# Optimization experiments

Measured on AMD Instinct MI355X. Metric: run time of the kernel, lower is better.

Reference implementation:

```python
import jax, jax.numpy as jnp
import numpy as np

B, N, C, K = 2, 4096, 256, 64


def setup_inputs() -> dict:
    key = jax.random.key(0)
    k1, k2, k3, k4, k5, k6 = jax.random.split(key, 6)
    points = jax.random.normal(k1, (B, N, 3), dtype=jnp.float32)  # ~N(0,1) cloud
    point_features = jax.random.normal(k2, (B, N, C), dtype=jnp.float32)
    # proposals: centers inside the cloud, positive box dims, random yaw (unused by mask math)
    centers = jax.random.uniform(k3, (B, K, 3), minval=-1.0, maxval=1.0, dtype=jnp.float32)
    dims = jax.random.uniform(k4, (B, K, 3), minval=0.5, maxval=1.5, dtype=jnp.float32)
    ry = jax.random.uniform(k5, (B, K, 1), minval=-np.pi, maxval=np.pi, dtype=jnp.float32)
    proposals = jnp.concatenate([centers, dims, ry], axis=-1)  # (B,K,7)
    W1 = jax.random.normal(k6, (C, 256), dtype=jnp.float32) * (1.0 / np.sqrt(C))
    b1 = jnp.zeros((256,), dtype=jnp.float32)
    W2 = jax.random.normal(jax.random.fold_in(key, 7), (256, 256), dtype=jnp.float32) * (1.0 / 16.0)
    b2 = jnp.zeros((256,), dtype=jnp.float32)
    return {"points": points, "point_features": point_features, "proposals": proposals,
            "W1": W1, "b1": b1, "W2": W2, "b2": b2}


def reference(points, point_features, proposals, W1, b1, W2, b2):
    # points: (B,N,3), point_features: (B,N,C), proposals: (B,K,7)
    ctr = proposals[..., :3]                      # (B,K,3) cx,cy,cz
    half = proposals[..., 3:6] * 0.5              # (B,K,3) l/2,w/2,h/2
    lo = ctr - half                               # (B,K,3)
    hi = ctr + half
    # point-in-box mask (axis-aligned, strict inequalities as in source): (B,K,N)
    p = points[:, None, :, :]                     # (B,1,N,3)
    mask = jnp.all((p > lo[:, :, None, :]) & (p < hi[:, :, None, :]), axis=-1)
    any_in = jnp.any(mask, axis=-1)               # (B,K)
    # masked max-pool over points: (B,K,N,C) -> (B,K,C)
    neg_inf = jnp.asarray(-jnp.inf, point_features.dtype)
    masked = jnp.where(mask[..., None], point_features[:, None, :, :], neg_inf)
    pooled = jnp.max(masked, axis=2)
    pooled = jnp.where(any_in[..., None], pooled, 0.0)  # empty box -> zeros
    # fc: Linear(C,256) + ReLU + Linear(256,256) + ReLU
    h = jax.nn.relu(jnp.einsum('bkc,cd->bkd', pooled, W1) + b1)
    out = jax.nn.relu(jnp.einsum('bkd,de->bke', h, W2) + b2)
    return out
```

## Files before the change

### kernel.cpp

```cpp
#include <hip/hip_runtime.h>

#define Bn 2
#define Nn 4096
#define Cn 256
#define Kn 64
#define BK (Bn * Kn)
#define NSEG 8
#define SEGN (Nn / NSEG)
#define NB1 (BK * NSEG)
#define W1T 4
#define PAD1 (7 * W1T)

__device__ __forceinline__ float4 max4(float4 a, float4 b) {
    return make_float4(fmaxf(a.x, b.x), fmaxf(a.y, b.y),
                       fmaxf(a.z, b.z), fmaxf(a.w, b.w));
}

__global__ __launch_bounds__(256) void pool_seg_kernel(
    const float* __restrict__ points,
    const float* __restrict__ feats,
    const float* __restrict__ proposals,
    float* __restrict__ partial)
{
    const int blk  = blockIdx.x;
    const int bk   = blk >> 3;
    const int seg  = blk & 7;
    const int b    = bk / Kn;
    const int tid  = threadIdx.x;
    const int w    = tid >> 6;
    const int lane = tid & 63;

    __shared__ int   s_idx[SEGN + PAD1];
    __shared__ int   s_count;
    __shared__ float s_part[W1T][Cn];

    const float* prop = proposals + (size_t)bk * 7;
    const float cx = prop[0], cy = prop[1], cz = prop[2];
    const float hx = prop[3] * 0.5f, hy = prop[4] * 0.5f, hz = prop[5] * 0.5f;
    const float lox = cx - hx, loy = cy - hy, loz = cz - hz;
    const float hix = cx + hx, hiy = cy + hy, hiz = cz + hz;

    if (tid == 0) s_count = 0;
    __syncthreads();

    if (tid < 128) {
        const int n0 = seg * SEGN + 4 * tid;
        const float4* pv = (const float4*)(points + (size_t)b * Nn * 3
                                           + (size_t)seg * SEGN * 3);
        const float4 q0 = pv[3 * tid + 0];
        const float4 q1 = pv[3 * tid + 1];
        const float4 q2 = pv[3 * tid + 2];

        const bool in0 = (q0.x > lox) & (q0.x < hix) &
                         (q0.y > loy) & (q0.y < hiy) &
                         (q0.z > loz) & (q0.z < hiz);
        const bool in1 = (q0.w > lox) & (q0.w < hix) &
                         (q1.x > loy) & (q1.x < hiy) &
                         (q1.y > loz) & (q1.y < hiz);
        const bool in2 = (q1.z > lox) & (q1.z < hix) &
                         (q1.w > loy) & (q1.w < hiy) &
                         (q2.x > loz) & (q2.x < hiz);
        const bool in3 = (q2.y > lox) & (q2.y < hix) &
                         (q2.z > loy) & (q2.z < hiy) &
                         (q2.w > loz) & (q2.w < hiz);

        const unsigned long long m0 = __ballot(in0);
        const unsigned long long m1 = __ballot(in1);
        const unsigned long long m2 = __ballot(in2);
        const unsigned long long m3 = __ballot(in3);
        const int c0 = __popcll(m0), c1 = __popcll(m1);
        const int c2 = __popcll(m2), c3 = __popcll(m3);

        int base = 0;
        if (lane == 0) base = atomicAdd(&s_count, c0 + c1 + c2 + c3);
        base = __shfl(base, 0);

        const unsigned long long below = (lane == 63)
            ? 0xFFFFFFFFFFFFFFFFull >> 1
            : ((1ull << lane) - 1);
        if (in0) s_idx[base + __popcll(m0 & below)] = n0 + 0;
        if (in1) s_idx[base + c0 + __popcll(m1 & below)] = n0 + 1;
        if (in2) s_idx[base + c0 + c1 + __popcll(m2 & below)] = n0 + 2;
        if (in3) s_idx[base + c0 + c1 + c2 + __popcll(m3 & below)] = n0 + 3;
    }
    __syncthreads();
    const int count = s_count;

    if (count > 0 && tid < PAD1) s_idx[count + tid] = s_idx[0];
    __syncthreads();

    const float* fb = feats + (size_t)b * Nn * Cn;
    float4 mx = make_float4(-INFINITY, -INFINITY, -INFINITY, -INFINITY);
    for (int i = w; i < count; i += 8 * W1T) {
        const int a0 = s_idx[i + 0 * W1T], a1 = s_idx[i + 1 * W1T];
        const int a2 = s_idx[i + 2 * W1T], a3 = s_idx[i + 3 * W1T];
        const int a4 = s_idx[i + 4 * W1T], a5 = s_idx[i + 5 * W1T];
        const int a6 = s_idx[i + 6 * W1T], a7 = s_idx[i + 7 * W1T];
        const float4 f0 = *(const float4*)(fb + (size_t)a0 * Cn + lane * 4);
        const float4 f1 = *(const float4*)(fb + (size_t)a1 * Cn + lane * 4);
        const float4 f2 = *(const float4*)(fb + (size_t)a2 * Cn + lane * 4);
        const float4 f3 = *(const float4*)(fb + (size_t)a3 * Cn + lane * 4);
        const float4 f4 = *(const float4*)(fb + (size_t)a4 * Cn + lane * 4);
        const float4 f5 = *(const float4*)(fb + (size_t)a5 * Cn + lane * 4);
        const float4 f6 = *(const float4*)(fb + (size_t)a6 * Cn + lane * 4);
        const float4 f7 = *(const float4*)(fb + (size_t)a7 * Cn + lane * 4);
        mx = max4(mx, max4(max4(f0, f1), max4(f2, f3)));
        mx = max4(mx, max4(max4(f4, f5), max4(f6, f7)));
    }
    *(float4*)&s_part[w][lane * 4] = mx;
    __syncthreads();

    {
        float m = fmaxf(fmaxf(s_part[0][tid], s_part[1][tid]),
                        fmaxf(s_part[2][tid], s_part[3][tid]));
        partial[(size_t)blk * Cn + tid] = m;
    }
}

__global__ __launch_bounds__(1024) void reduce_mlp_kernel(
    const float* __restrict__ partial,
    const float* __restrict__ W1,
    const float* __restrict__ b1,
    const float* __restrict__ W2,
    const float* __restrict__ b2,
    float* __restrict__ out)
{
    const int bk  = blockIdx.x;
    const int tid = threadIdx.x;
    const int g   = tid >> 8;
    const int d   = tid & 255;

    __shared__ float s_m[4][Cn];
    __shared__ float s_vec[Cn];
    __shared__ float s_red[4][Cn];

    {
        const float* pp = partial + ((size_t)bk * NSEG) * Cn + d;
        const float a = pp[(size_t)(2 * g + 0) * Cn];
        const float c = pp[(size_t)(2 * g + 1) * Cn];
        s_m[g][d] = fmaxf(a, c);
    }
    __syncthreads();

    if (tid < Cn) {
        float m = fmaxf(fmaxf(s_m[0][tid], s_m[1][tid]),
                        fmaxf(s_m[2][tid], s_m[3][tid]));
        if (m == -INFINITY) m = 0.0f;
        s_vec[tid] = m;
    }
    __syncthreads();

    {
        const float* w1 = W1 + (size_t)(g * 64) * 256 + d;
        const float* sv = s_vec + g * 64;
        float acc = 0.0f;
        #pragma unroll 16
        for (int c = 0; c < 64; ++c)
            acc = fmaf(sv[c], w1[(size_t)c * 256], acc);
        s_red[g][d] = acc;
    }
    __syncthreads();
    if (tid < Cn) {
        s_vec[tid] = fmaxf(
            b1[tid] + ((s_red[0][tid] + s_red[1][tid]) +
                       (s_red[2][tid] + s_red[3][tid])), 0.0f);
    }
    __syncthreads();

    {
        const float* w2 = W2 + (size_t)(g * 64) * 256 + d;
        const float* sv = s_vec + g * 64;
        float acc = 0.0f;
        #pragma unroll 16
        for (int c = 0; c < 64; ++c)
            acc = fmaf(sv[c], w2[(size_t)c * 256], acc);
        s_red[g][d] = acc;
    }
    __syncthreads();
    if (tid < Cn) {
        out[(size_t)bk * 256 + tid] = fmaxf(
            b2[tid] + ((s_red[0][tid] + s_red[1][tid]) +
                       (s_red[2][tid] + s_red[3][tid])), 0.0f);
    }
}

extern "C" void kernel_launch(void* const* d_in, const int* in_sizes, int n_in,
                              void* d_out, int out_size, void* d_ws, size_t ws_size,
                              hipStream_t stream) {
    const float* points    = (const float*)d_in[0];
    const float* feats     = (const float*)d_in[1];
    const float* proposals = (const float*)d_in[2];
    const float* W1        = (const float*)d_in[3];
    const float* b1        = (const float*)d_in[4];
    const float* W2        = (const float*)d_in[5];
    const float* b2        = (const float*)d_in[6];
    float* out             = (float*)d_out;
    float* partial         = (float*)d_ws;

    pool_seg_kernel<<<NB1, 256, 0, stream>>>(points, feats, proposals,
                                             partial);
    reduce_mlp_kernel<<<BK, 1024, 0, stream>>>(partial, W1, b1, W2, b2, out);
}
```

Before: 79.30 us.

## Fuse segment reduction and MLP into pooling kernel via last-block counter

Merges the two kernels into one. Each pooling block bumps a per-proposal atomic counter after writing its partial max, and the last of the eight segment blocks reduces the partials and runs both linear layers with 256 threads. This removes the second kernel launch and its dependency gap, at the cost of a memset launch, threadfence overhead, and a serial 256-long dot product per thread in the tail block.

```diff
diff --git a/kernel.cpp b/kernel.cpp
--- a/kernel.cpp
+++ b/kernel.cpp
@@ -16,11 +16,17 @@
                        fmaxf(a.z, b.z), fmaxf(a.w, b.w));
 }
 
-__global__ __launch_bounds__(256) void pool_seg_kernel(
+__global__ __launch_bounds__(256) void pool_seg_mlp_kernel(
     const float* __restrict__ points,
     const float* __restrict__ feats,
     const float* __restrict__ proposals,
-    float* __restrict__ partial)
+    const float* __restrict__ W1,
+    const float* __restrict__ b1,
+    const float* __restrict__ W2,
+    const float* __restrict__ b2,
+    float* __restrict__ out,
+    float* __restrict__ partial,
+    unsigned* __restrict__ counters)
 {
     const int blk  = blockIdx.x;
     const int bk   = blk >> 3;
@@ -33,6 +39,9 @@
     __shared__ int   s_idx[SEGN + PAD1];
     __shared__ int   s_count;
     __shared__ float s_part[W1T][Cn];
+    __shared__ float s_vec[Cn];
+    __shared__ float s_h[Cn];
+    __shared__ int   s_done;
 
     const float* prop = proposals + (size_t)bk * 7;
     const float cx = prop[0], cy = prop[1], cz = prop[2];
@@ -111,76 +120,41 @@
     __syncthreads();
 
     {
-        float m = fmaxf(fmaxf(s_part[0][tid], s_part[1][tid]),
-                        fmaxf(s_part[2][tid], s_part[3][tid]));
+        const float m = fmaxf(fmaxf(s_part[0][tid], s_part[1][tid]),
+                              fmaxf(s_part[2][tid], s_part[3][tid]));
         partial[(size_t)blk * Cn + tid] = m;
     }
-}
+    __threadfence();
+    if (tid == 0) s_done = (int)atomicAdd(&counters[bk], 1u);
+    __syncthreads();
+    if (s_done != NSEG - 1) return;
 
-__global__ __launch_bounds__(1024) void reduce_mlp_kernel(
-    const float* __restrict__ partial,
-    const float* __restrict__ W1,
-    const float* __restrict__ b1,
-    const float* __restrict__ W2,
-    const float* __restrict__ b2,
-    float* __restrict__ out)
-{
-    const int bk  = blockIdx.x;
-    const int tid = threadIdx.x;
-    const int g   = tid >> 8;
-    const int d   = tid & 255;
-
-    __shared__ float s_m[4][Cn];
-    __shared__ float s_vec[Cn];
-    __shared__ float s_red[4][Cn];
-
+    __threadfence();
     {
-        const float* pp = partial + ((size_t)bk * NSEG) * Cn + d;
-        const float a = pp[(size_t)(2 * g + 0) * Cn];
-        const float c = pp[(size_t)(2 * g + 1) * Cn];
-        s_m[g][d] = fmaxf(a, c);
-    }
-    __syncthreads();
-
-    if (tid < Cn) {
-        float m = fmaxf(fmaxf(s_m[0][tid], s_m[1][tid]),
-                        fmaxf(s_m[2][tid], s_m[3][tid]));
+        const float* pp = partial + (size_t)bk * NSEG * Cn + tid;
+        float m = pp[0];
+        #pragma unroll
+        for (int j = 1; j < NSEG; ++j) m = fmaxf(m, pp[(size_t)j * Cn]);
         if (m == -INFINITY) m = 0.0f;
         s_vec[tid] = m;
     }
     __syncthreads();
 
     {
-        const float* w1 = W1 + (size_t)(g * 64) * 256 + d;
-        const float* sv = s_vec + g * 64;
-        float acc = 0.0f;
+        float acc = b1[tid];
         #pragma unroll 16
-        for (int c = 0; c < 64; ++c)
-            acc = fmaf(sv[c], w1[(size_t)c * 256], acc);
-        s_red[g][d] = acc;
-    }
-    __syncthreads();
-    if (tid < Cn) {
-        s_vec[tid] = fmaxf(
-            b1[tid] + ((s_red[0][tid] + s_red[1][tid]) +
-                       (s_red[2][tid] + s_red[3][tid])), 0.0f);
+        for (int c = 0; c < Cn; ++c)
+            acc = fmaf(s_vec[c], W1[(size_t)c * 256 + tid], acc);
+        s_h[tid] = fmaxf(acc, 0.0f);
     }
     __syncthreads();
 
     {
-        const float* w2 = W2 + (size_t)(g * 64) * 256 + d;
-        const float* sv = s_vec + g * 64;
-        float acc = 0.0f;
+        float acc = b2[tid];
         #pragma unroll 16
-        for (int c = 0; c < 64; ++c)
-            acc = fmaf(sv[c], w2[(size_t)c * 256], acc);
-        s_red[g][d] = acc;
-    }
-    __syncthreads();
-    if (tid < Cn) {
-        out[(size_t)bk * 256 + tid] = fmaxf(
-            b2[tid] + ((s_red[0][tid] + s_red[1][tid]) +
-                       (s_red[2][tid] + s_red[3][tid])), 0.0f);
+        for (int c = 0; c < Cn; ++c)
+            acc = fmaf(s_h[c], W2[(size_t)c * 256 + tid], acc);
+        out[(size_t)bk * 256 + tid] = fmaxf(acc, 0.0f);
     }
 }
 
@@ -195,9 +169,13 @@
     const float* W2        = (const float*)d_in[5];
     const float* b2        = (const float*)d_in[6];
     float* out             = (float*)d_out;
-    float* partial         = (float*)d_ws;
 
-    pool_seg_kernel<<<NB1, 256, 0, stream>>>(points, feats, proposals,
-                                             partial);
-    reduce_mlp_kernel<<<BK, 1024, 0, stream>>>(partial, W1, b1, W2, b2, out);
+    float*    partial  = (float*)d_ws;
+    unsigned* counters = (unsigned*)((char*)d_ws + (size_t)NB1 * Cn * 4);
+
+    hipMemsetAsync(counters, 0, BK * sizeof(unsigned), stream);
+
+    pool_seg_mlp_kernel<<<NB1, 256, 0, stream>>>(points, feats, proposals,
+                                                 W1, b1, W2, b2, out,
+                                                 partial, counters);
 }
```

Measured after the change: 176.2 us. 2.22x slower.
